# Kernel tuning notes

Measured on AMD Instinct MI355X. Metric: run time of the kernel, lower is better.

The kernel has to match this reference:

```python
import jax, jax.numpy as jnp
import numpy as np

N = 100000   # nodes
E = 800000   # edges
H = 64       # hidden_channels (also input feature dim via lazy Linear)
OUT = 2      # out_channels
G = 64       # graphs in batch
EPS = 1e-5   # BatchNorm eps
N_PRE, N_CONV, N_POST = 3, 6, 3


def setup_inputs() -> dict:
    key = jax.random.key(0)
    ks = jax.random.split(key, 20)
    s = 0.1
    inp = {
        "x": jax.random.normal(ks[0], (N, H), jnp.float32),
        "edge_index": jax.random.randint(ks[1], (2, E), 0, N, dtype=jnp.int64),
        "batch": jnp.sort(jax.random.randint(ks[2], (N,), 0, G, dtype=jnp.int64)),
        # pre-processing MLP + BN params
        "pre_W": jax.random.normal(ks[3], (N_PRE, H, H), jnp.float32) * s,
        "pre_b": jax.random.normal(ks[4], (N_PRE, H), jnp.float32) * s,
        "pre_g": jnp.ones((N_PRE, H), jnp.float32),
        "pre_beta": jnp.zeros((N_PRE, H), jnp.float32),
        # GCNConv params (weight + bias per layer)
        "conv_W": jax.random.normal(ks[5], (N_CONV, H, H), jnp.float32) * s,
        "conv_b": jax.random.normal(ks[6], (N_CONV, H), jnp.float32) * s,
        # post-processing MLP + BN params
        "post_W": jax.random.normal(ks[7], (N_POST, H, H), jnp.float32) * s,
        "post_b": jax.random.normal(ks[8], (N_POST, H), jnp.float32) * s,
        "post_g": jnp.ones((N_POST, H), jnp.float32),
        "post_beta": jnp.zeros((N_POST, H), jnp.float32),
        # final head: H->H, H->H, H->OUT
        "fin_W0": jax.random.normal(ks[9], (H, H), jnp.float32) * s,
        "fin_b0": jax.random.normal(ks[10], (H,), jnp.float32) * s,
        "fin_W1": jax.random.normal(ks[11], (H, H), jnp.float32) * s,
        "fin_b1": jax.random.normal(ks[12], (H,), jnp.float32) * s,
        "fin_W2": jax.random.normal(ks[13], (H, OUT), jnp.float32) * s,
        "fin_b2": jax.random.normal(ks[14], (OUT,), jnp.float32) * s,
    }
    return inp


def _bn(h, g, b):
    # BatchNorm1d, training mode: biased batch statistics over node dim
    m = h.mean(0)
    v = h.var(0)
    return (h - m) * jax.lax.rsqrt(v + EPS) * g + b


def _gcn(h, src, dst, dinv, W, b):
    # PyG GCNConv: h' = D^-1/2 (A+I) D^-1/2 (h W) + b, sum-aggregated at dst
    hw = h @ W                                   # [N,H]
    norm = dinv[src] * dinv[dst]                 # [E]
    agg = jax.ops.segment_sum(hw[src] * norm[:, None], dst, num_segments=N)
    agg = agg + hw * (dinv * dinv)[:, None]      # self-loop contribution
    return agg + b


def reference(x, edge_index, batch, pre_W, pre_b, pre_g, pre_beta,
              conv_W, conv_b, post_W, post_b, post_g, post_beta,
              fin_W0, fin_b0, fin_W1, fin_b1, fin_W2, fin_b2):
    src, dst = edge_index[0], edge_index[1]
    # gcn_norm degree with self-loops (in-degree at dst), edge_weight = 1
    deg = jax.ops.segment_sum(jnp.ones((E,), x.dtype), dst, num_segments=N) + 1.0
    dinv = jax.lax.rsqrt(deg)

    h = x
    # pre-processing: Linear -> BN, relu except last
    for i in range(N_PRE):
        h = _bn(h @ pre_W[i] + pre_b[i], pre_g[i], pre_beta[i])
        if i != N_PRE - 1:
            h = jax.nn.relu(h)
    # GCNConv stack with residual adds
    for i in range(N_CONV):
        h = _gcn(h, src, dst, dinv, conv_W[i], conv_b[i]) + h
        if i != N_CONV - 1:
            h = jax.nn.relu(h)
    # post-processing: Linear -> BN, relu except last
    for i in range(N_POST):
        h = _bn(h @ post_W[i] + post_b[i], post_g[i], post_beta[i])
        if i != N_POST - 1:
            h = jax.nn.relu(h)
    # global_mean_pool over graphs
    counts = jax.ops.segment_sum(jnp.ones((N,), h.dtype), batch, num_segments=G)
    pooled = jax.ops.segment_sum(h, batch, num_segments=G) / jnp.maximum(counts, 1.0)[:, None]
    # final head (dropout is identity in eval)
    z = jax.nn.relu(pooled @ fin_W0 + fin_b0)
    z = jax.nn.relu(z @ fin_W1 + fin_b1)
    return z @ fin_W2 + fin_b2
```

## Files before the change

kernel.cpp:

```cpp
#include <hip/hip_runtime.h>

#define N_NODES 100000
#define N_EDGES 800000
#define HID 64
#define NGRAPH 64
#define OUTC 2
#define BN_EPS 1e-5f
#define NSCAN_BLK ((N_NODES + 255) / 256)
#define GEMM_BLK ((N_NODES + 63) / 64)
#define POOL_SUB 16

typedef __attribute__((ext_vector_type(8))) short bf16x8;
typedef __attribute__((ext_vector_type(4))) float f32x4;

__device__ __forceinline__ unsigned short f2bf(float f) {
    unsigned int u = __float_as_uint(f);
    u = (u + 0x7FFFu + ((u >> 16) & 1u)) >> 16;
    return (unsigned short)u;
}
__device__ __forceinline__ float bflo(unsigned int u) { return __uint_as_float(u << 16); }
__device__ __forceinline__ float bfhi(unsigned int u) { return __uint_as_float(u & 0xFFFF0000u); }
__device__ __forceinline__ unsigned int bfpack(float a, float b) {
    return (unsigned int)f2bf(a) | ((unsigned int)f2bf(b) << 16);
}

template <int IN_MODE, bool IN_FP32, bool ADD_BIAS, bool ROW_SCALE, bool STATS>
__global__ __launch_bounds__(256) void k_gemm(const void* __restrict__ Xv,
                                              const float* __restrict__ W,
                                              const float* __restrict__ bias,
                                              const float* __restrict__ dinv,
                                              const float* __restrict__ scsh,
                                              unsigned short* __restrict__ Y,
                                              float* __restrict__ partial, int n) {
    __shared__ __align__(16) unsigned short sXb[64][72];
    __shared__ __align__(16) unsigned short sWT[64][72];
    __shared__ float sDinv[64];
    const int tid  = threadIdx.x;
    const int row0 = blockIdx.x * 64;

    #pragma unroll
    for (int i = tid; i < 1024; i += 256) {
        int k = i >> 4, c4 = (i & 15) << 2;
        float4 w = *reinterpret_cast<const float4*>(&W[k * 64 + c4]);
        sWT[c4 + 0][k] = f2bf(w.x);
        sWT[c4 + 1][k] = f2bf(w.y);
        sWT[c4 + 2][k] = f2bf(w.z);
        sWT[c4 + 3][k] = f2bf(w.w);
    }
    if (IN_FP32) {
        const float* X = (const float*)Xv;
        #pragma unroll
        for (int f = tid; f < 1024; f += 256) {
            int r = f >> 4, c4 = (f & 15) << 2;
            float4 v = make_float4(0.f, 0.f, 0.f, 0.f);
            if (row0 + r < n)
                v = *reinterpret_cast<const float4*>(&X[(size_t)(row0 + r) * HID + c4]);
            if (IN_MODE >= 1) {
                float4 sc = *reinterpret_cast<const float4*>(&scsh[c4]);
                float4 sh = *reinterpret_cast<const float4*>(&scsh[64 + c4]);
                v.x = v.x * sc.x + sh.x; v.y = v.y * sc.y + sh.y;
                v.z = v.z * sc.z + sh.z; v.w = v.w * sc.w + sh.w;
                if (IN_MODE == 2) {
                    v.x = fmaxf(v.x, 0.f); v.y = fmaxf(v.y, 0.f);
                    v.z = fmaxf(v.z, 0.f); v.w = fmaxf(v.w, 0.f);
                }
            }
            sXb[r][c4 + 0] = f2bf(v.x);
            sXb[r][c4 + 1] = f2bf(v.y);
            sXb[r][c4 + 2] = f2bf(v.z);
            sXb[r][c4 + 3] = f2bf(v.w);
        }
    } else {
        const unsigned short* X = (const unsigned short*)Xv;
        #pragma unroll
        for (int f = tid; f < 512; f += 256) {
            int r = f >> 3, c8 = (f & 7) << 3;
            uint4 u = make_uint4(0u, 0u, 0u, 0u);
            if (row0 + r < n)
                u = *reinterpret_cast<const uint4*>(&X[(size_t)(row0 + r) * HID + c8]);
            if (IN_MODE >= 1) {
                float v[8];
                v[0] = bflo(u.x); v[1] = bfhi(u.x);
                v[2] = bflo(u.y); v[3] = bfhi(u.y);
                v[4] = bflo(u.z); v[5] = bfhi(u.z);
                v[6] = bflo(u.w); v[7] = bfhi(u.w);
                #pragma unroll
                for (int k = 0; k < 8; ++k) {
                    v[k] = v[k] * scsh[c8 + k] + scsh[64 + c8 + k];
                    if (IN_MODE == 2) v[k] = fmaxf(v[k], 0.f);
                }
                u.x = bfpack(v[0], v[1]); u.y = bfpack(v[2], v[3]);
                u.z = bfpack(v[4], v[5]); u.w = bfpack(v[6], v[7]);
            }
            *reinterpret_cast<uint4*>(&sXb[r][c8]) = u;
        }
    }
    if (ROW_SCALE && tid < 64)
        sDinv[tid] = (row0 + tid < n) ? dinv[row0 + tid] : 0.f;
    __syncthreads();

    const int lane = tid & 63;
    const int wv   = tid >> 6;
    const int cl   = lane & 15;
    const int kg   = lane >> 4;
    const int col  = (wv << 4) + cl;

    const f32x4 zero = {0.f, 0.f, 0.f, 0.f};
    f32x4 acc[4];
    #pragma unroll
    for (int m = 0; m < 4; ++m) acc[m] = zero;

    #pragma unroll
    for (int k0 = 0; k0 < 64; k0 += 32) {
        bf16x8 bfrag = *reinterpret_cast<const bf16x8*>(&sWT[col][k0 + (kg << 3)]);
        #pragma unroll
        for (int m = 0; m < 4; ++m) {
            bf16x8 afrag = *reinterpret_cast<const bf16x8*>(&sXb[(m << 4) + cl][k0 + (kg << 3)]);
            acc[m] = __builtin_amdgcn_mfma_f32_16x16x32_bf16(afrag, bfrag, acc[m], 0, 0, 0);
        }
    }

    const float bb = ADD_BIAS ? bias[col] : 0.f;
    float colS = 0.f, colQ = 0.f;
    #pragma unroll
    for (int m = 0; m < 4; ++m) {
        #pragma unroll
        for (int j = 0; j < 4; ++j) {
            int rl = (m << 4) + (kg << 2) + j;
            int r  = row0 + rl;
            if (r < n) {
                float s = ROW_SCALE ? sDinv[rl] : 1.f;
                float o = acc[m][j] * s + bb;
                Y[(size_t)r * HID + col] = f2bf(o);
                if (STATS) { colS += o; colQ += o * o; }
            }
        }
    }
    if (STATS) {
        colS += __shfl_xor(colS, 16); colQ += __shfl_xor(colQ, 16);
        colS += __shfl_xor(colS, 32); colQ += __shfl_xor(colQ, 32);
        if (kg == 0) {
            partial[blockIdx.x * 128 + col]      = colS;
            partial[blockIdx.x * 128 + 64 + col] = colQ;
        }
    }
}

__global__ __launch_bounds__(256) void k_statsfin(const float* __restrict__ partial,
                                                  const float* __restrict__ g,
                                                  const float* __restrict__ beta,
                                                  float* __restrict__ scsh, int n) {
    int c = blockIdx.x, t = threadIdx.x;
    float S = 0.f, Q = 0.f;
    for (int b = t; b < GEMM_BLK; b += 256) {
        S += partial[b * 128 + c];
        Q += partial[b * 128 + 64 + c];
    }
    __shared__ float ss[256], sq[256];
    ss[t] = S; sq[t] = Q;
    __syncthreads();
    for (int off = 128; off > 0; off >>= 1) {
        if (t < off) { ss[t] += ss[t + off]; sq[t] += sq[t + off]; }
        __syncthreads();
    }
    if (t == 0) {
        float nf = (float)n;
        float m  = ss[0] / nf;
        float v  = sq[0] / nf - m * m;
        float sc = rsqrtf(v + BN_EPS) * g[c];
        scsh[c]      = sc;
        scsh[64 + c] = beta[c] - m * sc;
    }
}

__global__ __launch_bounds__(256) void k_deg(const int* __restrict__ dst,
                                             int* __restrict__ indeg) {
    int e = blockIdx.x * 256 + threadIdx.x;
    if (e < N_EDGES) atomicAdd(&indeg[dst[e]], 1);
}

__global__ __launch_bounds__(256) void k_scanpart(const int* __restrict__ indeg,
                                                  int* __restrict__ bsum) {
    __shared__ int s[256];
    int i = blockIdx.x * 256 + threadIdx.x;
    s[threadIdx.x] = (i < N_NODES) ? indeg[i] : 0;
    __syncthreads();
    for (int off = 128; off > 0; off >>= 1) {
        if (threadIdx.x < off) s[threadIdx.x] += s[threadIdx.x + off];
        __syncthreads();
    }
    if (threadIdx.x == 0) bsum[blockIdx.x] = s[0];
}

__global__ __launch_bounds__(512) void k_scanmid(int* __restrict__ bsum, int nblk) {
    __shared__ int s[512];
    int t = threadIdx.x;
    int v = (t < nblk) ? bsum[t] : 0;
    s[t] = v;
    __syncthreads();
    for (int off = 1; off < 512; off <<= 1) {
        int x = (t >= off) ? s[t - off] : 0;
        __syncthreads();
        s[t] += x;
        __syncthreads();
    }
    if (t < nblk) bsum[t] = s[t] - v;
}

__global__ __launch_bounds__(256) void k_scanfinal(const int* __restrict__ indeg,
                                                   const int* __restrict__ bsum,
                                                   int* __restrict__ rowptr,
                                                   float* __restrict__ dinv) {
    __shared__ int s[256];
    int t = threadIdx.x;
    int i = blockIdx.x * 256 + t;
    int v = (i < N_NODES) ? indeg[i] : 0;
    s[t] = v;
    __syncthreads();
    for (int off = 1; off < 256; off <<= 1) {
        int x = (t >= off) ? s[t - off] : 0;
        __syncthreads();
        s[t] += x;
        __syncthreads();
    }
    if (i < N_NODES) {
        rowptr[i] = bsum[blockIdx.x] + s[t] - v;
        dinv[i]   = rsqrtf((float)v + 1.f);
    }
    if (i == 0) rowptr[N_NODES] = N_EDGES;
}

__global__ __launch_bounds__(256) void k_fill(const int* __restrict__ src,
                                              const int* __restrict__ dst,
                                              const int* __restrict__ rowptr,
                                              int* __restrict__ indeg,
                                              int* __restrict__ colidx) {
    int e = blockIdx.x * 256 + threadIdx.x;
    if (e >= N_EDGES) return;
    int d = dst[e];
    int pos = rowptr[d] + (atomicSub(&indeg[d], 1) - 1);
    colidx[pos] = src[e];
}

template <int IN_MODE, bool RELU>
__global__ __launch_bounds__(256) void k_gather(const int* __restrict__ rowptr,
                                                const int* __restrict__ colidx,
                                                const unsigned short* __restrict__ HWb,
                                                const unsigned short* __restrict__ Hin,
                                                const float* __restrict__ dinv,
                                                const float* __restrict__ bias,
                                                const float* __restrict__ scsh,
                                                unsigned short* __restrict__ Out) {
    int d = blockIdx.x * 4 + (threadIdx.x >> 6);
    if (d >= N_NODES) return;
    const int lane = threadIdx.x & 63;
    const int slot = lane >> 3;
    const int c8   = (lane & 7) << 3;
    const int j0 = rowptr[d], j1 = rowptr[d + 1];

    float acc[8];
    #pragma unroll
    for (int k = 0; k < 8; ++k) acc[k] = 0.f;

    if (slot == 7) {
        uint4 v = *reinterpret_cast<const uint4*>(&HWb[(size_t)d * HID + c8]);
        acc[0] += bflo(v.x); acc[1] += bfhi(v.x);
        acc[2] += bflo(v.y); acc[3] += bfhi(v.y);
        acc[4] += bflo(v.z); acc[5] += bfhi(v.z);
        acc[6] += bflo(v.w); acc[7] += bfhi(v.w);
    }
    for (int j = j0 + slot; j < j1; j += 8) {
        int s = colidx[j];
        uint4 v = *reinterpret_cast<const uint4*>(&HWb[(size_t)s * HID + c8]);
        acc[0] += bflo(v.x); acc[1] += bfhi(v.x);
        acc[2] += bflo(v.y); acc[3] += bfhi(v.y);
        acc[4] += bflo(v.z); acc[5] += bfhi(v.z);
        acc[6] += bflo(v.w); acc[7] += bfhi(v.w);
    }
    #pragma unroll
    for (int m = 8; m < 64; m <<= 1) {
        #pragma unroll
        for (int k = 0; k < 8; ++k) acc[k] += __shfl_xor(acc[k], m);
    }

    if (slot == 0) {
        uint4 hv = *reinterpret_cast<const uint4*>(&Hin[(size_t)d * HID + c8]);
        float h[8];
        h[0] = bflo(hv.x); h[1] = bfhi(hv.x);
        h[2] = bflo(hv.y); h[3] = bfhi(hv.y);
        h[4] = bflo(hv.z); h[5] = bfhi(hv.z);
        h[6] = bflo(hv.w); h[7] = bfhi(hv.w);
        if (IN_MODE == 1) {
            #pragma unroll
            for (int k = 0; k < 8; ++k)
                h[k] = h[k] * scsh[c8 + k] + scsh[64 + c8 + k];
        }
        float di = dinv[d];
        float o[8];
        #pragma unroll
        for (int k = 0; k < 8; ++k) {
            o[k] = acc[k] * di + bias[c8 + k] + h[k];
            if (RELU) o[k] = fmaxf(o[k], 0.f);
        }
        uint4 ov;
        ov.x = bfpack(o[0], o[1]); ov.y = bfpack(o[2], o[3]);
        ov.z = bfpack(o[4], o[5]); ov.w = bfpack(o[6], o[7]);
        *reinterpret_cast<uint4*>(&Out[(size_t)d * HID + c8]) = ov;
    }
}

__device__ __forceinline__ int lowerb(const int* __restrict__ b, int n, int v) {
    int lo = 0, hi = n;
    while (lo < hi) { int m = (lo + hi) >> 1; if (b[m] < v) lo = m + 1; else hi = m; }
    return lo;
}

__global__ __launch_bounds__(256) void k_pool1(const unsigned short* __restrict__ Y,
                                               const int* __restrict__ batch,
                                               float* __restrict__ partial2) {
    int g  = blockIdx.x >> 4;
    int sb = blockIdx.x & 15;
    int tid = threadIdx.x, col = tid & 63, rg = tid >> 6;
    int lo = lowerb(batch, N_NODES, g);
    int hi = lowerb(batch, N_NODES, g + 1);
    int cnt = hi - lo;
    int st = lo + (int)(((long long)cnt * sb) >> 4);
    int en = lo + (int)(((long long)cnt * (sb + 1)) >> 4);
    float s = 0.f;
    for (int r = st + rg; r < en; r += 4)
        s += bflo((unsigned int)Y[(size_t)r * HID + col]);
    __shared__ float ls[4][64];
    ls[rg][col] = s;
    __syncthreads();
    if (tid < 64)
        partial2[(size_t)blockIdx.x * 64 + tid] =
            ls[0][tid] + ls[1][tid] + ls[2][tid] + ls[3][tid];
}

__global__ __launch_bounds__(256) void k_final(const float* __restrict__ partial2,
                                               const int* __restrict__ batch,
                                               const float* __restrict__ scsh,
                                               const float* __restrict__ W0,
                                               const float* __restrict__ b0,
                                               const float* __restrict__ W1,
                                               const float* __restrict__ b1,
                                               const float* __restrict__ W2,
                                               const float* __restrict__ b2,
                                               float* __restrict__ out) {
    __shared__ float P[64][65];
    __shared__ float Z[64][65];
    __shared__ int sOff[NGRAPH + 1];
    int tid = threadIdx.x;
    if (tid <= NGRAPH) sOff[tid] = lowerb(batch, N_NODES, tid);
    __syncthreads();
    for (int i = tid; i < NGRAPH * HID; i += 256) {
        int g = i >> 6, c = i & 63;
        float S = 0.f;
        #pragma unroll
        for (int sb = 0; sb < POOL_SUB; ++sb)
            S += partial2[(size_t)(g * POOL_SUB + sb) * 64 + c];
        int cnt = sOff[g + 1] - sOff[g];
        float v = 0.f;
        if (cnt > 0) v = (S / (float)cnt) * scsh[c] + scsh[64 + c];
        P[g][c] = v;
    }
    __syncthreads();
    for (int t = 0; t < 16; ++t) {
        int o = tid + 256 * t; int r = o >> 6, c = o & 63;
        float acc = b0[c];
        #pragma unroll 8
        for (int k = 0; k < 64; ++k) acc += P[r][k] * W0[k * 64 + c];
        Z[r][c] = fmaxf(acc, 0.f);
    }
    __syncthreads();
    for (int t = 0; t < 16; ++t) {
        int o = tid + 256 * t; int r = o >> 6, c = o & 63;
        float acc = b1[c];
        #pragma unroll 8
        for (int k = 0; k < 64; ++k) acc += Z[r][k] * W1[k * 64 + c];
        P[r][c] = fmaxf(acc, 0.f);
    }
    __syncthreads();
    if (tid < NGRAPH * OUTC) {
        int r = tid >> 1, c = tid & 1;
        float acc = b2[c];
        #pragma unroll 8
        for (int k = 0; k < 64; ++k) acc += P[r][k] * W2[k * OUTC + c];
        out[tid] = acc;
    }
}

extern "C" void kernel_launch(void* const* d_in, const int* in_sizes, int n_in,
                              void* d_out, int out_size, void* d_ws, size_t ws_size,
                              hipStream_t stream) {
    const float* x        = (const float*)d_in[0];
    const int*   ei       = (const int*)d_in[1];
    const int*   batch    = (const int*)d_in[2];
    const float* pre_W    = (const float*)d_in[3];
    const float* pre_b    = (const float*)d_in[4];
    const float* pre_g    = (const float*)d_in[5];
    const float* pre_beta = (const float*)d_in[6];
    const float* conv_W   = (const float*)d_in[7];
    const float* conv_b   = (const float*)d_in[8];
    const float* post_W   = (const float*)d_in[9];
    const float* post_b   = (const float*)d_in[10];
    const float* post_g   = (const float*)d_in[11];
    const float* post_beta= (const float*)d_in[12];
    const float* fW0 = (const float*)d_in[13];
    const float* fb0 = (const float*)d_in[14];
    const float* fW1 = (const float*)d_in[15];
    const float* fb1 = (const float*)d_in[16];
    const float* fW2 = (const float*)d_in[17];
    const float* fb2 = (const float*)d_in[18];
    float* out = (float*)d_out;

    const size_t NH = (size_t)N_NODES * HID;
    float* ws       = (float*)d_ws;
    float* A        = ws;
    float* B        = A + NH;
    float* C        = B + NH;
    float* dinv     = C + NH;
    float* partial  = dinv + N_NODES;
    float* scsh     = partial + (size_t)GEMM_BLK*128;
    float* partial2 = scsh + 6 * 128;
    int*   indeg    = (int*)(partial2 + NGRAPH * POOL_SUB * 64);
    int*   rowptr   = indeg + N_NODES;
    int*   colidx   = rowptr + N_NODES + 1;
    int*   bsum     = colidx + N_EDGES;
    unsigned short* Ab  = (unsigned short*)A;
    unsigned short* Bb  = (unsigned short*)B;
    unsigned short* Cb  = (unsigned short*)C;

    const int* srcp = ei;
    const int* dstp = ei + N_EDGES;

    const int gEdge  = (N_EDGES + 255) / 256;
    const int gNode4 = (N_NODES + 3) / 4;

    hipMemsetAsync(indeg, 0, N_NODES * sizeof(int), stream);
    k_deg<<<gEdge, 256, 0, stream>>>(dstp, indeg);
    k_scanpart<<<NSCAN_BLK, 256, 0, stream>>>(indeg, bsum);
    k_scanmid<<<1, 512, 0, stream>>>(bsum, NSCAN_BLK);
    k_scanfinal<<<NSCAN_BLK, 256, 0, stream>>>(indeg, bsum, rowptr, dinv);
    k_fill<<<gEdge, 256, 0, stream>>>(srcp, dstp, rowptr, indeg, colidx);

    k_gemm<0, true,  true, false, true><<<GEMM_BLK, 256, 0, stream>>>(x, pre_W, pre_b, nullptr, nullptr, Ab, partial, N_NODES);
    k_statsfin<<<64, 256, 0, stream>>>(partial, pre_g, pre_beta, scsh + 0 * 128, N_NODES);

    k_gemm<2, false, true, false, true><<<GEMM_BLK, 256, 0, stream>>>(Ab, pre_W + 4096, pre_b + 64, nullptr, scsh + 0 * 128, Cb, partial, N_NODES);
    k_statsfin<<<64, 256, 0, stream>>>(partial, pre_g + 64, pre_beta + 64, scsh + 1 * 128, N_NODES);

    k_gemm<2, false, true, false, true><<<GEMM_BLK, 256, 0, stream>>>(Cb, pre_W + 2 * 4096, pre_b + 128, nullptr, scsh + 1 * 128, Ab, partial, N_NODES);
    k_statsfin<<<64, 256, 0, stream>>>(partial, pre_g + 128, pre_beta + 128, scsh + 2 * 128, N_NODES);

    for (int i = 0; i < 6; ++i) {
        const unsigned short* in = (i & 1) ? Cb : Ab;
        unsigned short*     outb = (i & 1) ? Ab : Cb;
        const float* Wl = conv_W + i * 4096;
        const float* bl = conv_b + i * 64;
        if (i == 0)
            k_gemm<1, false, false, true, false><<<GEMM_BLK, 256, 0, stream>>>(in, Wl, nullptr, dinv, scsh + 2 * 128, Bb, nullptr, N_NODES);
        else
            k_gemm<0, false, false, true, false><<<GEMM_BLK, 256, 0, stream>>>(in, Wl, nullptr, dinv, nullptr, Bb, nullptr, N_NODES);

        if (i == 0)
            k_gather<1, true ><<<gNode4, 256, 0, stream>>>(rowptr, colidx, Bb, in, dinv, bl, scsh + 2 * 128, outb);
        else if (i != 5)
            k_gather<0, true ><<<gNode4, 256, 0, stream>>>(rowptr, colidx, Bb, in, dinv, bl, nullptr, outb);
        else
            k_gather<0, false><<<gNode4, 256, 0, stream>>>(rowptr, colidx, Bb, in, dinv, bl, nullptr, outb);
    }

    k_gemm<0, false, true, false, true><<<GEMM_BLK, 256, 0, stream>>>(Ab, post_W, post_b, nullptr, nullptr, Cb, partial, N_NODES);
    k_statsfin<<<64, 256, 0, stream>>>(partial, post_g, post_beta, scsh + 3 * 128, N_NODES);

    k_gemm<2, false, true, false, true><<<GEMM_BLK, 256, 0, stream>>>(Cb, post_W + 4096, post_b + 64, nullptr, scsh + 3 * 128, Ab, partial, N_NODES);
    k_statsfin<<<64, 256, 0, stream>>>(partial, post_g + 64, post_beta + 64, scsh + 4 * 128, N_NODES);

    k_gemm<2, false, true, false, true><<<GEMM_BLK, 256, 0, stream>>>(Ab, post_W + 2 * 4096, post_b + 128, nullptr, scsh + 4 * 128, Cb, partial, N_NODES);
    k_statsfin<<<64, 256, 0, stream>>>(partial, post_g + 128, post_beta + 128, scsh + 5 * 128, N_NODES);

    k_pool1<<<NGRAPH * POOL_SUB, 256, 0, stream>>>(Cb, batch, partial2);
    k_final<<<1, 256, 0, stream>>>(partial2, batch, scsh + 5 * 128,
                                   fW0, fb0, fW1, fb1, fW2, fb2, out);
}
```

Before: 573.3 us.

## Build CSR via two-level bucket sort with shared-memory atomics

Replaces the global-atomic degree count, three-kernel scan, and atomic fill with a bucketed counting sort. Edges are first histogrammed per 2048-node bucket, scanned, and scattered into bucket-contiguous order. A per-bucket kernel then builds rowptr, dinv and colidx using shared-memory atomics. This removes random global atomics and one memset, but adds an extra pass over the edges through an int2 scratch array and reduces parallelism in the CSR stage to 49 blocks.

```diff
diff --git a/kernel.cpp b/kernel.cpp
--- a/kernel.cpp
+++ b/kernel.cpp
@@ -6,9 +6,12 @@
 #define NGRAPH 64
 #define OUTC 2
 #define BN_EPS 1e-5f
-#define NSCAN_BLK ((N_NODES + 255) / 256)
 #define GEMM_BLK ((N_NODES + 63) / 64)
 #define POOL_SUB 16
+#define BSHIFT 11
+#define NBUCK 64
+#define NBUCK_ACT ((N_NODES + (1 << BSHIFT) - 1) >> BSHIFT)
+#define NEB_BLK ((N_EDGES + 2047) / 2048)
 
 typedef __attribute__((ext_vector_type(8))) short bf16x8;
 typedef __attribute__((ext_vector_type(4))) float f32x4;
@@ -173,73 +176,131 @@
     }
 }
 
-__global__ __launch_bounds__(256) void k_deg(const int* __restrict__ dst,
-                                             int* __restrict__ indeg) {
-    int e = blockIdx.x * 256 + threadIdx.x;
-    if (e < N_EDGES) atomicAdd(&indeg[dst[e]], 1);
-}
-
-__global__ __launch_bounds__(256) void k_scanpart(const int* __restrict__ indeg,
-                                                  int* __restrict__ bsum) {
-    __shared__ int s[256];
-    int i = blockIdx.x * 256 + threadIdx.x;
-    s[threadIdx.x] = (i < N_NODES) ? indeg[i] : 0;
-    __syncthreads();
-    for (int off = 128; off > 0; off >>= 1) {
-        if (threadIdx.x < off) s[threadIdx.x] += s[threadIdx.x + off];
+__global__ __launch_bounds__(256) void k_hist(const int* __restrict__ dst,
+                                              int* __restrict__ histmat) {
+    __shared__ int lh[NBUCK];
+    int t = threadIdx.x;
+    if (t < NBUCK) lh[t] = 0;
+    __syncthreads();
+    int base = blockIdx.x * 2048;
+    for (int i = t; i < 2048; i += 256) {
+        int e = base + i;
+        if (e < N_EDGES) atomicAdd(&lh[dst[e] >> BSHIFT], 1);
+    }
+    __syncthreads();
+    if (t < NBUCK) histmat[blockIdx.x * NBUCK + t] = lh[t];
+}
+
+__global__ __launch_bounds__(256) void k_escan(const int* __restrict__ histmat,
+                                               int* __restrict__ blockoff,
+                                               int* __restrict__ bucketbase) {
+    __shared__ int csum[4][NBUCK];
+    __shared__ int cbase[4][NBUCK];
+    __shared__ int tot[NBUCK + 1];
+    int t = threadIdx.x;
+    int b = t & 63, c = t >> 6;
+    const int CHUNK = (NEB_BLK + 3) / 4;
+    int lo = c * CHUNK, hi = min(lo + CHUNK, NEB_BLK);
+    int s = 0;
+    #pragma unroll 8
+    for (int blk = lo; blk < hi; ++blk) s += histmat[blk * NBUCK + b];
+    csum[c][b] = s;
+    __syncthreads();
+    if (t < NBUCK) {
+        int r = 0;
+        #pragma unroll
+        for (int c2 = 0; c2 < 4; ++c2) { cbase[c2][t] = r; r += csum[c2][t]; }
+        tot[t] = r;
+    }
+    __syncthreads();
+    if (t == 0) {
+        int r = 0;
+        for (int b2 = 0; b2 < NBUCK; ++b2) { int v = tot[b2]; tot[b2] = r; r += v; }
+        tot[NBUCK] = r;
+    }
+    __syncthreads();
+    if (t <= NBUCK) bucketbase[t] = tot[t];
+    int r = cbase[c][b];
+    #pragma unroll 8
+    for (int blk = lo; blk < hi; ++blk) {
+        blockoff[blk * NBUCK + b] = r;
+        r += histmat[blk * NBUCK + b];
+    }
+}
+
+__global__ __launch_bounds__(256) void k_reorder(const int* __restrict__ src,
+                                                 const int* __restrict__ dst,
+                                                 const int* __restrict__ blockoff,
+                                                 const int* __restrict__ bucketbase,
+                                                 int2* __restrict__ esort) {
+    __shared__ int lcur[NBUCK];
+    int t = threadIdx.x;
+    if (t < NBUCK) lcur[t] = 0;
+    __syncthreads();
+    int base = blockIdx.x * 2048;
+    for (int i = t; i < 2048; i += 256) {
+        int e = base + i;
+        if (e < N_EDGES) {
+            int d = dst[e];
+            int b = d >> BSHIFT;
+            int r = atomicAdd(&lcur[b], 1);
+            esort[bucketbase[b] + blockoff[blockIdx.x * NBUCK + b] + r] =
+                make_int2(src[e], d);
+        }
+    }
+}
+
+__global__ __launch_bounds__(256) void k_csr(const int2* __restrict__ esort,
+                                             const int* __restrict__ bucketbase,
+                                             int* __restrict__ rowptr,
+                                             int* __restrict__ colidx,
+                                             float* __restrict__ dinv) {
+    __shared__ int lh[1 << BSHIFT];
+    __shared__ int ctot[256];
+    int t = threadIdx.x;
+    int b = blockIdx.x;
+    int node0 = b << BSHIFT;
+    int nNodes = min(1 << BSHIFT, N_NODES - node0);
+    int e0 = bucketbase[b], e1 = bucketbase[b + 1];
+    #pragma unroll
+    for (int i = t; i < (1 << BSHIFT); i += 256) lh[i] = 0;
+    __syncthreads();
+    for (int e = e0 + t; e < e1; e += 256)
+        atomicAdd(&lh[esort[e].y - node0], 1);
+    __syncthreads();
+    int c0 = t * 8;
+    int cnt[8];
+    int s = 0;
+    #pragma unroll
+    for (int j = 0; j < 8; ++j) { cnt[j] = lh[c0 + j]; s += cnt[j]; }
+    ctot[t] = s;
+    __syncthreads();
+    int v = ctot[t];
+    for (int off = 1; off < 256; off <<= 1) {
+        int x = (t >= off) ? ctot[t - off] : 0;
         __syncthreads();
-    }
-    if (threadIdx.x == 0) bsum[blockIdx.x] = s[0];
-}
-
-__global__ __launch_bounds__(512) void k_scanmid(int* __restrict__ bsum, int nblk) {
-    __shared__ int s[512];
-    int t = threadIdx.x;
-    int v = (t < nblk) ? bsum[t] : 0;
-    s[t] = v;
-    __syncthreads();
-    for (int off = 1; off < 512; off <<= 1) {
-        int x = (t >= off) ? s[t - off] : 0;
+        ctot[t] += x;
         __syncthreads();
-        s[t] += x;
-        __syncthreads();
-    }
-    if (t < nblk) bsum[t] = s[t] - v;
-}
-
-__global__ __launch_bounds__(256) void k_scanfinal(const int* __restrict__ indeg,
-                                                   const int* __restrict__ bsum,
-                                                   int* __restrict__ rowptr,
-                                                   float* __restrict__ dinv) {
-    __shared__ int s[256];
-    int t = threadIdx.x;
-    int i = blockIdx.x * 256 + t;
-    int v = (i < N_NODES) ? indeg[i] : 0;
-    s[t] = v;
-    __syncthreads();
-    for (int off = 1; off < 256; off <<= 1) {
-        int x = (t >= off) ? s[t - off] : 0;
-        __syncthreads();
-        s[t] += x;
-        __syncthreads();
-    }
-    if (i < N_NODES) {
-        rowptr[i] = bsum[blockIdx.x] + s[t] - v;
-        dinv[i]   = rsqrtf((float)v + 1.f);
-    }
-    if (i == 0) rowptr[N_NODES] = N_EDGES;
-}
-
-__global__ __launch_bounds__(256) void k_fill(const int* __restrict__ src,
-                                              const int* __restrict__ dst,
-                                              const int* __restrict__ rowptr,
-                                              int* __restrict__ indeg,
-                                              int* __restrict__ colidx) {
-    int e = blockIdx.x * 256 + threadIdx.x;
-    if (e >= N_EDGES) return;
-    int d = dst[e];
-    int pos = rowptr[d] + (atomicSub(&indeg[d], 1) - 1);
-    colidx[pos] = src[e];
+    }
+    int run = ctot[t] - v;
+    #pragma unroll
+    for (int j = 0; j < 8; ++j) {
+        int idx = c0 + j;
+        int cv = cnt[j];
+        lh[idx] = run;
+        if (idx < nNodes) {
+            rowptr[node0 + idx] = e0 + run;
+            dinv[node0 + idx]   = rsqrtf((float)cv + 1.f);
+        }
+        run += cv;
+    }
+    __syncthreads();
+    for (int e = e0 + t; e < e1; e += 256) {
+        int2 ed = esort[e];
+        int r = atomicAdd(&lh[ed.y - node0], 1);
+        colidx[e0 + r] = ed.x;
+    }
+    if (b == 0 && t == 0) rowptr[N_NODES] = N_EDGES;
 }
 
 template <int IN_MODE, bool RELU>
@@ -415,34 +476,30 @@
     float* out = (float*)d_out;
 
     const size_t NH = (size_t)N_NODES * HID;
-    float* ws       = (float*)d_ws;
-    float* A        = ws;
-    float* B        = A + NH;
-    float* C        = B + NH;
-    float* dinv     = C + NH;
+    unsigned short* Ab = (unsigned short*)d_ws;
+    unsigned short* Bb = Ab + NH;
+    unsigned short* Cb = Bb + NH;
+    float* dinv     = (float*)(Cb + NH);
     float* partial  = dinv + N_NODES;
     float* scsh     = partial + (size_t)GEMM_BLK*128;
     float* partial2 = scsh + 6 * 128;
-    int*   indeg    = (int*)(partial2 + NGRAPH * POOL_SUB * 64);
-    int*   rowptr   = indeg + N_NODES;
-    int*   colidx   = rowptr + N_NODES + 1;
-    int*   bsum     = colidx + N_EDGES;
-    unsigned short* Ab  = (unsigned short*)A;
-    unsigned short* Bb  = (unsigned short*)B;
-    unsigned short* Cb  = (unsigned short*)C;
+    int* histmat    = (int*)(partial2 + NGRAPH * POOL_SUB * 64);
+    int* blockoff   = histmat + NEB_BLK * NBUCK;
+    int* bucketbase = blockoff + NEB_BLK * NBUCK;
+    int* rowptr     = bucketbase + NBUCK + 1;
+    int* colidx     = rowptr + N_NODES + 1;
+    size_t eoff = (size_t)(colidx + N_EDGES - (int*)d_ws);
+    eoff = (eoff + 1) & ~(size_t)1;
+    int2* esort     = (int2*)((int*)d_ws + eoff);
 
     const int* srcp = ei;
     const int* dstp = ei + N_EDGES;
-
-    const int gEdge  = (N_EDGES + 255) / 256;
     const int gNode4 = (N_NODES + 3) / 4;
 
-    hipMemsetAsync(indeg, 0, N_NODES * sizeof(int), stream);
-    k_deg<<<gEdge, 256, 0, stream>>>(dstp, indeg);
-    k_scanpart<<<NSCAN_BLK, 256, 0, stream>>>(indeg, bsum);
-    k_scanmid<<<1, 512, 0, stream>>>(bsum, NSCAN_BLK);
-    k_scanfinal<<<NSCAN_BLK, 256, 0, stream>>>(indeg, bsum, rowptr, dinv);
-    k_fill<<<gEdge, 256, 0, stream>>>(srcp, dstp, rowptr, indeg, colidx);
+    k_hist<<<NEB_BLK, 256, 0, stream>>>(dstp, histmat);
+    k_escan<<<1, 256, 0, stream>>>(histmat, blockoff, bucketbase);
+    k_reorder<<<NEB_BLK, 256, 0, stream>>>(srcp, dstp, blockoff, bucketbase, esort);
+    k_csr<<<NBUCK_ACT, 256, 0, stream>>>(esort, bucketbase, rowptr, colidx, dinv);
 
     k_gemm<0, true,  true, false, true><<<GEMM_BLK, 256, 0, stream>>>(x, pre_W, pre_b, nullptr, nullptr, Ab, partial, N_NODES);
     k_statsfin<<<64, 256, 0, stream>>>(partial, pre_g, pre_beta, scsh + 0 * 128, N_NODES);
```

Measured after the change: 534.4 us. 6.8% less time.
